# Kernel tuning notes

Measured on AMD Instinct MI355X. Metric: run time of the kernel, lower is better.

Reference implementation:

```python
import jax, jax.numpy as jnp
import numpy as np

# RoIAlign 2D config (matches init_kwargs)
OUT_H, OUT_W = 7, 7
SPATIAL_SCALE = 0.25
S = 2  # sampling_ratio: S x S sample points per output bin
N, C, H, W = 4, 256, 200, 200
R = 512


def setup_inputs() -> dict:
    key = jax.random.key(0)
    k1, k2, k3, k4, k5 = jax.random.split(key, 5)
    features = jax.random.normal(k1, (N, C, H, W), dtype=jnp.float32)
    # rois in image coordinates (image is H/scale = 800 px): (batch_idx, x1, y1, x2, y2)
    img = H / SPATIAL_SCALE
    b = jax.random.randint(k2, (R,), 0, N).astype(jnp.float32)
    xy1 = jax.random.uniform(k3, (R, 2), dtype=jnp.float32, maxval=img - 96.0)
    wh = jax.random.uniform(k4, (R, 2), dtype=jnp.float32, minval=16.0, maxval=96.0)
    rois = jnp.concatenate([b[:, None], xy1, xy1 + wh], axis=1)  # [R,5]
    return {"features": features, "rois": rois}


def _axis_weights(start, bin_size, out_size, limit):
    """Per-axis sample coords -> (low/high indices [R,out*S,2], lerp weights [R,out*S,2]).
    Matches mmdet/torchvision RoIAlign CUDA kernel semantics."""
    # sample coordinate: start + (i + 0.5) * bin / S  ==  start + ph*bin + (iy+0.5)*bin/S
    i = (jnp.arange(out_size * S, dtype=jnp.float32) + 0.5) / S
    y = start[:, None] + i[None, :] * bin_size[:, None]          # [R, out*S]
    valid = (y >= -1.0) & (y <= limit)                            # kernel: skip if y<-1 or y>H
    yc = jnp.clip(y, 0.0, limit - 1.0)
    yl = jnp.floor(yc).astype(jnp.int32)                          # in [0, H-1]
    yh = jnp.minimum(yl + 1, limit - 1)
    l = yc - yl.astype(jnp.float32)                               # 0 at the top edge, as in kernel
    w = jnp.stack([1.0 - l, l], axis=-1) * valid[..., None].astype(jnp.float32)  # [R,out*S,2]
    idx = jnp.stack([yl, yh], axis=-1)                            # [R,out*S,2]
    return idx, w


def reference(features, rois):
    # order=1 (bilinear) path of RoIAlign2DFunction
    b = rois[:, 0].astype(jnp.int32)                              # [R]
    x1, y1, x2, y2 = (rois[:, k] * SPATIAL_SCALE for k in (1, 2, 3, 4))
    roi_w = jnp.maximum(x2 - x1, 1.0)
    roi_h = jnp.maximum(y2 - y1, 1.0)
    bin_w = roi_w / OUT_W
    bin_h = roi_h / OUT_H

    yidx, wy = _axis_weights(y1, bin_h, OUT_H, H)                 # [R,Hs,2]
    xidx, wx = _axis_weights(x1, bin_w, OUT_W, W)                 # [R,Ws,2]

    nhwc = jnp.transpose(features, (0, 2, 3, 1))                  # [N,H,W,C]
    # gather 2x2 bilinear neighbors for every sample point: [R,Hs,Ws,2,2,C]
    vals = nhwc[b[:, None, None, None, None],
                yidx[:, :, None, :, None],
                xidx[:, None, :, None, :]]
    samples = jnp.einsum('rhwabc,rha,rwb->rhwc', vals, wy, wx)    # [R,Hs,Ws,C]
    Hs, Ws = OUT_H * S, OUT_W * S
    pooled = samples.reshape(R, OUT_H, S, OUT_W, S, C).mean(axis=(2, 4))  # avg over S*S points
    return jnp.transpose(pooled, (0, 3, 1, 2))                    # [R,C,out_h,out_w]
```

## Files before the change

kernel.cpp:

```cpp
#include <hip/hip_runtime.h>


#define OH 7
#define OW 7
#define NSAMP 14
#define NB 4
#define CH 256
#define FH 200
#define FW 200
#define NR 512
#define CCH 8
#define NCHUNK (CH / CCH)
#define MAXF 25
#define PSTRMAX (MAXF * 32 + 4)
#define BLK 256

__global__ __launch_bounds__(NR) void roi_sort(
    const float* __restrict__ rois, int* __restrict__ perm)
{
    __shared__ unsigned key[NR];
    const int t = threadIdx.x;
    {
        const int   b  = (int)rois[t * 5 + 0];
        const float x1 = rois[t * 5 + 1] * 0.25f;
        const float y1 = rois[t * 5 + 2] * 0.25f;
        const int qy = min(255, max(0, (int)y1));
        const int qx = min(255, max(0, (int)x1));
        key[t] = ((unsigned)b << 27) | ((unsigned)qy << 18)
               | ((unsigned)qx << 9) | (unsigned)t;
    }
    for (int k = 2; k <= NR; k <<= 1) {
        for (int j = k >> 1; j > 0; j >>= 1) {
            __syncthreads();
            const int ixj = t ^ j;
            if (ixj > t) {
                const unsigned a = key[t], c = key[ixj];
                const bool asc = ((t & k) == 0);
                if ((a > c) == asc) { key[t] = c; key[ixj] = a; }
            }
        }
    }
    __syncthreads();
    perm[t] = (int)(key[t] & (NR - 1u));
}

__global__ __launch_bounds__(BLK) void roialign_fwd(
    const float* __restrict__ feat,
    const float* __restrict__ rois,
    const int*   __restrict__ perm,
    float* __restrict__ out)
{
    __shared__ float tile[CCH * PSTRMAX];
    __shared__ int   s_il[2][NSAMP];
    __shared__ int   s_ih[2][NSAMP];
    __shared__ float s_w0[2][NSAMP];
    __shared__ float s_w1[2][NSAMP];

    const int bid   = blockIdx.x;
    const int nid   = ((bid & 7) << 11) | (bid >> 3);
    const int chunk = nid >> 9;
    const int r     = perm[nid & (NR - 1)];
    const int c0    = chunk * CCH;
    const int tid   = threadIdx.x;

    const int   b  = (int)rois[r * 5 + 0];
    const float x1 = rois[r * 5 + 1] * 0.25f;
    const float y1 = rois[r * 5 + 2] * 0.25f;
    const float x2 = rois[r * 5 + 3] * 0.25f;
    const float y2 = rois[r * 5 + 4] * 0.25f;
    const float roi_w = fmaxf(x2 - x1, 1.0f);
    const float roi_h = fmaxf(y2 - y1, 1.0f);
    const float bw = roi_w * (1.0f / OW);
    const float bh = roi_h * (1.0f / OH);

    if (tid < 2 * NSAMP) {
        const int axis = tid >= NSAMP;
        const int i    = tid - axis * NSAMP;
        const float start = axis ? x1 : y1;
        const float bsz   = axis ? bw : bh;
        const float pos   = start + (i + 0.5f) * 0.5f * bsz;
        const float valid = (pos >= -1.0f && pos <= 200.0f) ? 1.0f : 0.0f;
        const float pc    = fminf(fmaxf(pos, 0.0f), 199.0f);
        const int   il    = (int)floorf(pc);
        const int   ih    = min(il + 1, 199);
        const float l     = pc - (float)il;
        s_il[axis][i] = il;
        s_ih[axis][i] = ih;
        s_w0[axis][i] = (1.0f - l) * valid;
        s_w1[axis][i] = l * valid;
    }
    __syncthreads();

    const int ylo = s_il[0][0];
    const int xlo = s_il[1][0];
    const int fh = min(s_ih[0][NSAMP - 1] - ylo + 1, MAXF);
    const int fw = min(s_ih[1][NSAMP - 1] - xlo + 1, MAXF);
    const int x0   = xlo & ~3;
    const int nseg = ((xlo - x0) + fw + 3) >> 2;
    const int pstr = (fh << 5) + 4;

    {
        const int lane = tid & 63;
        const int wave = tid >> 6;
        const float* gend = feat + (size_t)NB * CH * FH * FW - 4;
        #pragma unroll
        for (int k = 0; k < 2; k++) {
            const int c = (wave << 1) | k;
            const float* gplane =
                feat + ((size_t)(b * CH + c0 + c) * FH + ylo) * FW + x0;
            float* lplane = tile + c * pstr;
            #pragma unroll
            for (int t = 0; t < 4; t++) {
                const int s  = (t << 6) + lane;
                const int ys = s >> 3;
                const int sx = s & 7;
                if (ys < fh && sx < nseg) {
                    const float* g = gplane + ys * FW + (sx << 2);
                    if (g > gend) g = gend;
                    __builtin_amdgcn_global_load_lds(
                        (const __attribute__((address_space(1))) void*)g,
                        (__attribute__((address_space(3))) void*)(lplane + (s << 2)),
                        16, 0, 0);
                }
            }
        }
    }
    __syncthreads();

    const int cl   = tid & (CCH - 1);
    const int slot = tid >> 3;
    const float* tc = tile + cl * pstr;

    for (int bin = slot; bin < OH * OW; bin += BLK / CCH) {
        const int ph = bin / OW;
        const int pw = bin - ph * OW;
        float acc = 0.0f;
        #pragma unroll
        for (int sy = 0; sy < 2; sy++) {
            const int gy = ph * 2 + sy;
            const int rowl = (s_il[0][gy] - ylo) << 5;
            const int rowh = (s_ih[0][gy] - ylo) << 5;
            const float wy0 = s_w0[0][gy];
            const float wy1 = s_w1[0][gy];
            #pragma unroll
            for (int sx = 0; sx < 2; sx++) {
                const int gx = pw * 2 + sx;
                const int ixl = s_il[1][gx] - x0;
                const int ixh = s_ih[1][gx] - x0;
                const float wx0 = s_w0[1][gx];
                const float wx1 = s_w1[1][gx];
                acc += wy0 * (wx0 * tc[rowl + ixl] + wx1 * tc[rowl + ixh])
                     + wy1 * (wx0 * tc[rowh + ixl] + wx1 * tc[rowh + ixh]);
            }
        }
        out[(size_t)(r * CH + c0 + cl) * (OH * OW) + bin] = acc * 0.25f;
    }
}

extern "C" void kernel_launch(void* const* d_in, const int* in_sizes, int n_in,
                              void* d_out, int out_size, void* d_ws, size_t ws_size,
                              hipStream_t stream) {
    const float* feat = (const float*)d_in[0];
    const float* rois = (const float*)d_in[1];
    float* out = (float*)d_out;
    int* perm = (int*)d_ws;
    roi_sort<<<1, NR, 0, stream>>>(rois, perm);
    roialign_fwd<<<NR * NCHUNK, BLK, 0, stream>>>(feat, rois, perm, out);
}
```

Measured before the change: 242.3 us.

## Process eight ROI-chunk items per block with double-buffered LDS prefetch

Each block now handles eight consecutive work items instead of one, launching 2048 blocks in place of 16384. Sample coordinates for all eight items are computed up front, using shuffles to derive the footprint bounds. The global-to-LDS tile for the next item is issued while the current one is computed from a second buffer. This is meant to hide global load latency and amortise block setup, at the cost of doubled LDS per block (lower occupancy), fewer blocks to spread across CUs, and a barrier per item.

```diff
diff --git a/kernel.cpp b/kernel.cpp
--- a/kernel.cpp
+++ b/kernel.cpp
@@ -10,9 +10,11 @@
 #define FW 200
 #define NR 512
 #define CCH 8
-#define NCHUNK (CH / CCH)
 #define MAXF 25
-#define PSTRMAX (MAXF * 32 + 4)
+#define PSTR 804
+#define BUFSTR (CCH * PSTR)
+#define NIT 8
+#define GRID 2048
 #define BLK 256
 
 __global__ __launch_bounds__(NR) void roi_sort(
@@ -50,71 +52,82 @@
     const int*   __restrict__ perm,
     float* __restrict__ out)
 {
-    __shared__ float tile[CCH * PSTRMAX];
-    __shared__ int   s_il[2][NSAMP];
-    __shared__ int   s_ih[2][NSAMP];
-    __shared__ float s_w0[2][NSAMP];
-    __shared__ float s_w1[2][NSAMP];
+    __shared__ float tile[2 * BUFSTR];
+    __shared__ int   s_ilih[NIT][2][NSAMP];
+    __shared__ float s_w0[NIT][2][NSAMP];
+    __shared__ float s_w1[NIT][2][NSAMP];
+    __shared__ int4  s_item[NIT];
 
-    const int bid   = blockIdx.x;
-    const int nid   = ((bid & 7) << 11) | (bid >> 3);
-    const int chunk = nid >> 9;
-    const int r     = perm[nid & (NR - 1)];
-    const int c0    = chunk * CCH;
-    const int tid   = threadIdx.x;
+    const int tid = threadIdx.x;
+    const int bid = blockIdx.x;
+    const int nid_base = ((bid & 7) << 11) | ((bid >> 3) << 3);
 
-    const int   b  = (int)rois[r * 5 + 0];
-    const float x1 = rois[r * 5 + 1] * 0.25f;
-    const float y1 = rois[r * 5 + 2] * 0.25f;
-    const float x2 = rois[r * 5 + 3] * 0.25f;
-    const float y2 = rois[r * 5 + 4] * 0.25f;
-    const float roi_w = fmaxf(x2 - x1, 1.0f);
-    const float roi_h = fmaxf(y2 - y1, 1.0f);
-    const float bw = roi_w * (1.0f / OW);
-    const float bh = roi_h * (1.0f / OH);
-
-    if (tid < 2 * NSAMP) {
-        const int axis = tid >= NSAMP;
-        const int i    = tid - axis * NSAMP;
+    {
+        const int j  = tid >> 5;
+        const int k  = tid & 31;
+        const int kk = min(k, 27);
+        const int axis = (kk >= NSAMP) ? 1 : 0;
+        const int i    = kk - axis * NSAMP;
+        const int r  = perm[(nid_base + j) & (NR - 1)];
+        const int b  = (int)rois[r * 5 + 0];
+        const float x1 = rois[r * 5 + 1] * 0.25f;
+        const float y1 = rois[r * 5 + 2] * 0.25f;
+        const float x2 = rois[r * 5 + 3] * 0.25f;
+        const float y2 = rois[r * 5 + 4] * 0.25f;
+        const float rw = fmaxf(x2 - x1, 1.0f);
+        const float rh = fmaxf(y2 - y1, 1.0f);
+        const float bsz   = (axis ? rw : rh) * (1.0f / OW);
         const float start = axis ? x1 : y1;
-        const float bsz   = axis ? bw : bh;
         const float pos   = start + (i + 0.5f) * 0.5f * bsz;
         const float valid = (pos >= -1.0f && pos <= 200.0f) ? 1.0f : 0.0f;
         const float pc    = fminf(fmaxf(pos, 0.0f), 199.0f);
         const int   il    = (int)floorf(pc);
         const int   ih    = min(il + 1, 199);
         const float l     = pc - (float)il;
-        s_il[axis][i] = il;
-        s_ih[axis][i] = ih;
-        s_w0[axis][i] = (1.0f - l) * valid;
-        s_w1[axis][i] = l * valid;
+        if (k < 2 * NSAMP) {
+            s_ilih[j][axis][i] = il | (ih << 16);
+            s_w0[j][axis][i]   = (1.0f - l) * valid;
+            s_w1[j][axis][i]   = l * valid;
+        }
+        const int gb  = (tid & 63) & 32;
+        const int ylo = __shfl(il, gb + 0, 64);
+        const int yh  = __shfl(ih, gb + 13, 64);
+        const int xlo = __shfl(il, gb + 14, 64);
+        const int xh  = __shfl(ih, gb + 27, 64);
+        if (k == 0) {
+            const int fh   = min(yh - ylo + 1, MAXF);
+            const int fw   = min(xh - xlo + 1, MAXF);
+            const int x0   = xlo & ~3;
+            const int nseg = (xlo - x0 + fw + 3) >> 2;
+            s_item[j] = make_int4(ylo, x0, fh | (nseg << 8) | (b << 16), r);
+        }
     }
     __syncthreads();
 
-    const int ylo = s_il[0][0];
-    const int xlo = s_il[1][0];
-    const int fh = min(s_ih[0][NSAMP - 1] - ylo + 1, MAXF);
-    const int fw = min(s_ih[1][NSAMP - 1] - xlo + 1, MAXF);
-    const int x0   = xlo & ~3;
-    const int nseg = ((xlo - x0) + fw + 3) >> 2;
-    const int pstr = (fh << 5) + 4;
+    const int lane = tid & 63;
+    const int wave = tid >> 6;
+    const float* gend = feat + (size_t)NB * CH * FH * FW - 4;
 
-    {
-        const int lane = tid & 63;
-        const int wave = tid >> 6;
-        const float* gend = feat + (size_t)NB * CH * FH * FW - 4;
+    auto issue = [&](int j) {
+        const int4 si  = s_item[j];
+        const int ylo  = si.x, x0 = si.y;
+        const int fh   = si.z & 0xff;
+        const int nseg = (si.z >> 8) & 0xff;
+        const int b    = si.z >> 16;
+        const int c0   = ((nid_base + j) >> 9) << 3;
+        const float* fb =
+            feat + ((size_t)((b * CH + c0) * FH + ylo)) * FW + x0;
+        float* lbuf = tile + (j & 1) * BUFSTR;
         #pragma unroll
-        for (int k = 0; k < 2; k++) {
-            const int c = (wave << 1) | k;
-            const float* gplane =
-                feat + ((size_t)(b * CH + c0 + c) * FH + ylo) * FW + x0;
-            float* lplane = tile + c * pstr;
+        for (int kp = 0; kp < 2; kp++) {
+            const int c = (wave << 1) | kp;
+            const float* gplane = fb + (size_t)c * (FH * FW);
+            float* lplane = lbuf + c * PSTR;
             #pragma unroll
             for (int t = 0; t < 4; t++) {
                 const int s  = (t << 6) + lane;
-                const int ys = s >> 3;
-                const int sx = s & 7;
-                if (ys < fh && sx < nseg) {
+                const int ys = s >> 3, sx = s & 7;
+                if ((ys < fh) & (sx < nseg)) {
                     const float* g = gplane + ys * FW + (sx << 2);
                     if (g > gend) g = gend;
                     __builtin_amdgcn_global_load_lds(
@@ -124,37 +137,51 @@
                 }
             }
         }
+    };
+
+    auto compute = [&](int j) {
+        const int4 si = s_item[j];
+        const int ylo = si.x, x0 = si.y, r = si.w;
+        const int c0  = ((nid_base + j) >> 9) << 3;
+        const int cl  = tid & 7, slot = tid >> 3;
+        const float* tc = tile + (j & 1) * BUFSTR + cl * PSTR;
+        for (int bin = slot; bin < OH * OW; bin += 32) {
+            const int ph = bin / OW;
+            const int pw = bin - ph * OW;
+            float acc = 0.0f;
+            #pragma unroll
+            for (int sy = 0; sy < 2; sy++) {
+                const int gy  = ph * 2 + sy;
+                const int pky = s_ilih[j][0][gy];
+                const int rowl = ((pky & 0xffff) - ylo) << 5;
+                const int rowh = ((pky >> 16)    - ylo) << 5;
+                const float wy0 = s_w0[j][0][gy];
+                const float wy1 = s_w1[j][0][gy];
+                #pragma unroll
+                for (int sx2 = 0; sx2 < 2; sx2++) {
+                    const int gx  = pw * 2 + sx2;
+                    const int pkx = s_ilih[j][1][gx];
+                    const int ixl = (pkx & 0xffff) - x0;
+                    const int ixh = (pkx >> 16)    - x0;
+                    const float wx0 = s_w0[j][1][gx];
+                    const float wx1 = s_w1[j][1][gx];
+                    acc += wy0 * (wx0 * tc[rowl + ixl] + wx1 * tc[rowl + ixh])
+                         + wy1 * (wx0 * tc[rowh + ixl] + wx1 * tc[rowh + ixh]);
+                }
+            }
+            out[(size_t)(r * CH + c0 + cl) * (OH * OW) + bin] = acc * 0.25f;
+        }
+    };
+
+    issue(0);
+    __syncthreads();
+    #pragma unroll
+    for (int i = 0; i < NIT - 1; i++) {
+        issue(i + 1);
+        compute(i);
+        __syncthreads();
     }
-    __syncthreads();
-
-    const int cl   = tid & (CCH - 1);
-    const int slot = tid >> 3;
-    const float* tc = tile + cl * pstr;
-
-    for (int bin = slot; bin < OH * OW; bin += BLK / CCH) {
-        const int ph = bin / OW;
-        const int pw = bin - ph * OW;
-        float acc = 0.0f;
-        #pragma unroll
-        for (int sy = 0; sy < 2; sy++) {
-            const int gy = ph * 2 + sy;
-            const int rowl = (s_il[0][gy] - ylo) << 5;
-            const int rowh = (s_ih[0][gy] - ylo) << 5;
-            const float wy0 = s_w0[0][gy];
-            const float wy1 = s_w1[0][gy];
-            #pragma unroll
-            for (int sx = 0; sx < 2; sx++) {
-                const int gx = pw * 2 + sx;
-                const int ixl = s_il[1][gx] - x0;
-                const int ixh = s_ih[1][gx] - x0;
-                const float wx0 = s_w0[1][gx];
-                const float wx1 = s_w1[1][gx];
-                acc += wy0 * (wx0 * tc[rowl + ixl] + wx1 * tc[rowl + ixh])
-                     + wy1 * (wx0 * tc[rowh + ixl] + wx1 * tc[rowh + ixh]);
-            }
-        }
-        out[(size_t)(r * CH + c0 + cl) * (OH * OW) + bin] = acc * 0.25f;
-    }
+    compute(NIT - 1);
 }
 
 extern "C" void kernel_launch(void* const* d_in, const int* in_sizes, int n_in,
@@ -165,5 +192,5 @@
     float* out = (float*)d_out;
     int* perm = (int*)d_ws;
     roi_sort<<<1, NR, 0, stream>>>(rois, perm);
-    roialign_fwd<<<NR * NCHUNK, BLK, 0, stream>>>(feat, rois, perm, out);
+    roialign_fwd<<<GRID, BLK, 0, stream>>>(feat, rois, perm, out);
 }
```

New measurement: 268.2 us. 1.11x slower.
